# Performance work log

Measured on AMD Instinct MI355X. Metric: run time of the kernel, lower is better.

## Reference

```python
import jax, jax.numpy as jnp
import numpy as np

N_HEAD, D_MODEL, DQ, DK, DV = 16, 1024, 64, 64, 64
B, LQ, LK = 2, 2048, 2048
EPS = 1e-3


def setup_inputs() -> dict:
    key = jax.random.key(0)
    ks = jax.random.split(key, 8)
    v = jax.random.normal(ks[0], (B, LK, D_MODEL), jnp.float32)
    k = jax.random.normal(ks[1], (B, LK, D_MODEL), jnp.float32)
    q = jax.random.normal(ks[2], (B, LQ, D_MODEL), jnp.float32)
    mask = jax.random.randint(ks[3], (B, LQ, LK), 0, 2).astype(bool)
    # xavier_normal for [n_head, d_model, d*]: fan_in=d_model, fan_out=d* (per torch, last two dims)
    def xav(kk, shape):
        std = np.sqrt(2.0 / (shape[-2] + shape[-1]))
        return jax.random.normal(kk, shape, jnp.float32) * std
    w_q = xav(ks[4], (N_HEAD, D_MODEL, DQ))
    w_k = xav(ks[5], (N_HEAD, D_MODEL, DK))
    w_v = xav(ks[6], (N_HEAD, D_MODEL, DV))
    # output linear: torch default init; use uniform(-1/sqrt(fan_in), ..)
    fan_in = N_HEAD * DV
    bound = 1.0 / np.sqrt(fan_in)
    kw, kb = jax.random.split(ks[7])
    w_o = jax.random.uniform(kw, (fan_in, D_MODEL), jnp.float32, -bound, bound)
    b_o = jax.random.uniform(kb, (D_MODEL,), jnp.float32, -bound, bound)
    gamma = jnp.ones((D_MODEL,), jnp.float32)
    beta = jnp.zeros((D_MODEL,), jnp.float32)
    return {"v": v, "k": k, "q": q, "mask": mask, "w_q": w_q, "w_k": w_k,
            "w_v": w_v, "w_o": w_o, "b_o": b_o, "gamma": gamma, "beta": beta}


def _layer_norm(x, gamma, beta):
    mean = jnp.mean(x, axis=-1, keepdims=True)
    # torch.std default is unbiased (ddof=1); eps added to std (not var)
    std = jnp.std(x, axis=-1, keepdims=True, ddof=1)
    return (x - mean) / (std + EPS) * gamma + beta


def reference(v, k, q, mask, w_q, w_k, w_v, w_o, b_o, gamma, beta):
    residual = k  # source uses k as residual
    # per-head projections: [h, b, l, d*]
    qh = jnp.einsum('bld,hde->hble', q, w_q)
    kh = jnp.einsum('bld,hde->hble', k, w_k)
    vh = jnp.einsum('bld,hde->hble', v, w_v)
    scale = 1.0 / np.sqrt(DK)
    scores = jnp.einsum('hbqe,hbke->hbqk', qh, kh) * scale  # [h,b,Lq,Lk]
    scores = jnp.where(mask[None], -jnp.inf, scores)
    attn = jax.nn.softmax(scores, axis=-1)
    out = jnp.einsum('hbqk,hbke->hbqe', attn, vh)  # [h,b,Lq,dv]
    # cat(split(out, batch, dim=0), dim=-1): heads concatenated on last dim
    out = out.transpose(1, 2, 0, 3).reshape(out.shape[1], out.shape[2], -1)
    out = out @ w_o + b_o
    x = out + residual  # dropout is identity in eval
    return _layer_norm(x, gamma, beta)
```

## Files before the change

### kernel.cpp

```cpp
#include <hip/hip_runtime.h>
#include <math.h>

typedef __bf16 bf16_t;
typedef bf16_t bf16x8 __attribute__((ext_vector_type(8)));
typedef float  f32x4  __attribute__((ext_vector_type(4)));
typedef unsigned short u16;
typedef u16 ushortx4 __attribute__((ext_vector_type(4)));
typedef unsigned long long u64;

#define MFMA16(a, b, c) __builtin_amdgcn_mfma_f32_16x16x32_bf16((a), (b), (c), 0, 0, 0)

__device__ __forceinline__ u16 f2bf(float f) {
    unsigned int u = __float_as_uint(f);
    u = (u + 0x7fffu + ((u >> 16) & 1u)) >> 16;
    return (u16)u;
}

__device__ __forceinline__ float bf2f(unsigned int u) {
    return __uint_as_float(u << 16);
}

__device__ __forceinline__ void gld16(const u16* g, u16* l) {
    __builtin_amdgcn_global_load_lds(
        (const __attribute__((address_space(1))) void*)g,
        (__attribute__((address_space(3))) void*)l, 16, 0, 0);
}


__global__ __launch_bounds__(256) void k_cvt3(const float* __restrict__ q,
                                              const float* __restrict__ k,
                                              const float* __restrict__ v,
                                              u16* __restrict__ qb,
                                              u16* __restrict__ kb,
                                              u16* __restrict__ vb) {
    int i = blockIdx.x * 256 + threadIdx.x;
    int sel = blockIdx.y;
    const float* src = sel == 0 ? q : (sel == 1 ? k : v);
    u16* dst = sel == 0 ? qb : (sel == 1 ? kb : vb);
    float4 val = ((const float4*)src)[i];
    ushortx4 r;
    r[0] = f2bf(val.x); r[1] = f2bf(val.y); r[2] = f2bf(val.z); r[3] = f2bf(val.w);
    ((ushortx4*)dst)[i] = r;
}

__global__ __launch_bounds__(256) void k_tcvt3(const float* __restrict__ w_q,
                                               const float* __restrict__ w_k,
                                               const float* __restrict__ w_v,
                                               u16* __restrict__ wqt,
                                               u16* __restrict__ wkt,
                                               u16* __restrict__ wvt) {
    __shared__ float tile[32][33];
    int z = blockIdx.z, h = z & 15, sel = z >> 4;
    const float* src = (sel == 0 ? w_q : (sel == 1 ? w_k : w_v));
    u16* dst = (sel == 0 ? wqt : (sel == 1 ? wkt : wvt));
    int r0 = blockIdx.x * 32, c0 = blockIdx.y * 32;
    int tx = threadIdx.x & 31, ty = threadIdx.x >> 5;
    const float* s = src + ((size_t)h * 1024 + r0) * 64 + c0;
#pragma unroll
    for (int i = 0; i < 4; ++i) tile[ty + i * 8][tx] = s[(ty + i * 8) * 64 + tx];
    __syncthreads();
    u16* d = dst + ((size_t)h * 64 + c0) * 1024 + r0;
#pragma unroll
    for (int i = 0; i < 4; ++i) d[(ty + i * 8) * 1024 + tx] = f2bf(tile[tx][ty + i * 8]);
}

__global__ __launch_bounds__(256) void k_tcvt(const float* __restrict__ src,
                                              u16* __restrict__ dst, int R, int C) {
    __shared__ float tile[32][33];
    int r0 = blockIdx.x * 32, c0 = blockIdx.y * 32;
    int tx = threadIdx.x & 31, ty = threadIdx.x >> 5;
    const float* s = src + (size_t)r0 * C + c0;
#pragma unroll
    for (int i = 0; i < 4; ++i) tile[ty + i * 8][tx] = s[(ty + i * 8) * (size_t)C + tx];
    __syncthreads();
    u16* d = dst + (size_t)c0 * R + r0;
#pragma unroll
    for (int i = 0; i < 4; ++i) d[(ty + i * 8) * (size_t)R + tx] = f2bf(tile[tx][ty + i * 8]);
}

__global__ __launch_bounds__(256) void k_packmask(const int* __restrict__ mask,
                                                  u64* __restrict__ mask64) {
    int bid = blockIdx.x;
    int ktg = bid & 7, q4 = (bid >> 3) & 511, b = bid >> 12;
    int wave = threadIdx.x >> 6, lane = threadIdx.x & 63;
    int q = q4 * 4 + wave;
    const int* mp = mask + ((size_t)(b * 2048 + q)) * 2048 + ktg * 256 + lane;
#pragma unroll
    for (int i = 0; i < 4; ++i) {
        int m = mp[i * 64];
        u64 bal = __ballot(m != 0);
        if (lane == 0) mask64[((size_t)(b * 32 + ktg * 4 + i)) * 2048 + q] = bal;
    }
}

#define GEMM_CORE(Ablk, Bblk, ACC)                                                    \
    int c0 = wave * 2;                                                                \
    const u16* Ag0 = Ablk + (size_t)(c0 * 16 + l15) * 1024 + quad * 8;                \
    const u16* Ag1 = Ablk + (size_t)((c0 + 1) * 16 + l15) * 1024 + quad * 8;          \
    const u16* Bg0 = Bblk + (size_t)(c0 * 16 + l15) * 1024 + quad * 8;                \
    const u16* Bg1 = Bblk + (size_t)((c0 + 1) * 16 + l15) * 1024 + quad * 8;          \
    gld16(Ag0, As + c0 * 512); gld16(Ag1, As + (c0 + 1) * 512);                       \
    gld16(Bg0, Bs + c0 * 512); gld16(Bg1, Bs + (c0 + 1) * 512);                       \
    __syncthreads();                                                                  \
    int buf = 0;                                                                      \
    for (int ks = 0; ks < 32; ++ks) {                                                 \
        if (ks < 31) {                                                                \
            int k0 = (ks + 1) * 32;                                                   \
            gld16(Ag0 + k0, As + (buf ^ 1) * 4096 + c0 * 512);                        \
            gld16(Ag1 + k0, As + (buf ^ 1) * 4096 + (c0 + 1) * 512);                  \
            gld16(Bg0 + k0, Bs + (buf ^ 1) * 4096 + c0 * 512);                        \
            gld16(Bg1 + k0, Bs + (buf ^ 1) * 4096 + (c0 + 1) * 512);                  \
        }                                                                             \
        bf16x8 af[4], bfr[4];                                                         \
        _Pragma("unroll")                                                             \
        for (int i = 0; i < 4; ++i)                                                   \
            af[i] = *(const bf16x8*)(As + buf * 4096 + (wy * 4 + i) * 512 + lane * 8);\
        _Pragma("unroll")                                                             \
        for (int j = 0; j < 4; ++j)                                                   \
            bfr[j] = *(const bf16x8*)(Bs + buf * 4096 + (wx * 4 + j) * 512 + lane * 8);\
        _Pragma("unroll")                                                             \
        for (int i = 0; i < 4; ++i)                                                   \
            _Pragma("unroll")                                                         \
            for (int j = 0; j < 4; ++j) ACC[i][j] = MFMA16(af[i], bfr[j], ACC[i][j]); \
        __syncthreads();                                                              \
        buf ^= 1;                                                                     \
    }

__global__ __launch_bounds__(256) void k_proj(
    const u16* __restrict__ qb, const u16* __restrict__ kb, const u16* __restrict__ vb,
    const u16* __restrict__ wqt, const u16* __restrict__ wkt, const u16* __restrict__ wvt,
    u16* __restrict__ oq, u16* __restrict__ okh, u16* __restrict__ ovt) {
    __shared__ __align__(16) u16 smem[18432];
    u16* As = smem;
    u16* Bs = smem + 8192;
    int z = blockIdx.y, gx = blockIdx.x;
    int bm, bn;
    const u16 *A, *B;
    if (z == 0)      { bm = gx >> 3; bn = gx & 7; A = qb; B = wqt; }
    else if (z == 1) { bm = gx >> 3; bn = gx & 7; A = kb; B = wkt; }
    else             { bm = gx & 7; bn = gx >> 3; A = wvt; B = vb; }
    A += (size_t)bm * 128 * 1024;
    B += (size_t)bn * 128 * 1024;
    int tid = threadIdx.x, wave = tid >> 6, lane = tid & 63;
    int wy = wave >> 1, wx = wave & 1, l15 = lane & 15, quad = lane >> 4;
    f32x4 acc[4][4] = {};
    GEMM_CORE(A, B, acc)
    u16* ep = smem + wave * 4608;
    float mulf = (z == 0) ? 0.18033688011112042f : 1.0f;
#pragma unroll
    for (int i = 0; i < 4; ++i)
#pragma unroll
        for (int j = 0; j < 4; ++j)
#pragma unroll
            for (int r = 0; r < 4; ++r)
                ep[(i * 16 + quad * 4 + r) * 72 + j * 16 + l15] = f2bf(acc[i][j][r] * mulf);
    int rl = lane >> 3, cg = lane & 7;
    if (z < 2) {
        int hh = bn * 2 + wx;
        int m0 = bm * 128 + wy * 64;
        int bb = m0 >> 11, l0 = m0 & 2047;
        u16* O = (z ? okh : oq) + ((size_t)((hh * 2 + bb) * 2048 + l0)) * 64;
#pragma unroll
        for (int s = 0; s < 8; ++s) {
            int row = s * 8 + rl;
            uint4 v = *(const uint4*)(ep + row * 72 + cg * 8);
            *(uint4*)(O + (size_t)row * 64 + cg * 8) = v;
        }
    } else {
        int m0 = bm * 128 + wy * 64;
        int hh = m0 >> 6;
        int n0 = bn * 128 + wx * 64;
        int bb = n0 >> 11, l0 = n0 & 2047;
        u16* O = ovt + (size_t)(hh * 2 + bb) * 131072 + (size_t)(m0 & 63) * 2048 + l0;
#pragma unroll
        for (int s = 0; s < 8; ++s) {
            int row = s * 8 + rl;
            uint4 v = *(const uint4*)(ep + row * 72 + cg * 8);
            *(uint4*)(O + (size_t)row * 2048 + cg * 8) = v;
        }
    }
}

__global__ __launch_bounds__(512) void k_out(
    const u16* __restrict__ ao, const u16* __restrict__ wot,
    const float* __restrict__ bo, const float* __restrict__ resid,
    float* __restrict__ xb) {
    __shared__ __align__(16) u16 smem[18432];
    u16* As = smem;
    u16* Bs = smem + 8192;
    int gx = blockIdx.x, bm = gx >> 3, bn = gx & 7;
    const u16* A = ao + (size_t)bm * 128 * 1024;
    const u16* B = wot + (size_t)bn * 128 * 1024;
    int tid = threadIdx.x, wave = tid >> 6, lane = tid & 63;
    int wy = wave >> 2, wx = wave & 3, l15 = lane & 15, quad = lane >> 4;
    const u16* Ag = A + (size_t)(wave * 16 + l15) * 1024 + quad * 8;
    const u16* Bg = B + (size_t)(wave * 16 + l15) * 1024 + quad * 8;
    f32x4 acc[4][2] = {};
    gld16(Ag, As + wave * 512);
    gld16(Bg, Bs + wave * 512);
    __syncthreads();
    int buf = 0;
    for (int ks = 0; ks < 32; ++ks) {
        if (ks < 31) {
            int k0 = (ks + 1) * 32;
            gld16(Ag + k0, As + (buf ^ 1) * 4096 + wave * 512);
            gld16(Bg + k0, Bs + (buf ^ 1) * 4096 + wave * 512);
        }
        bf16x8 af[4], bfr[2];
#pragma unroll
        for (int i = 0; i < 4; ++i)
            af[i] = *(const bf16x8*)(As + buf * 4096 + (wy * 4 + i) * 512 + lane * 8);
#pragma unroll
        for (int j = 0; j < 2; ++j)
            bfr[j] = *(const bf16x8*)(Bs + buf * 4096 + (wx * 2 + j) * 512 + lane * 8);
#pragma unroll
        for (int i = 0; i < 4; ++i)
#pragma unroll
            for (int j = 0; j < 2; ++j) acc[i][j] = MFMA16(af[i], bfr[j], acc[i][j]);
        __syncthreads();
        buf ^= 1;
    }
    float* epf = (float*)smem + wave * 1152;
    int rl = lane >> 3, cg = lane & 7;
    int mbase = bm * 128 + wy * 64, nbase = bn * 128 + wx * 32;
#pragma unroll
    for (int cc = 0; cc < 2; ++cc) {
#pragma unroll
        for (int i2 = 0; i2 < 2; ++i2)
#pragma unroll
            for (int j = 0; j < 2; ++j)
#pragma unroll
                for (int r = 0; r < 4; ++r)
                    epf[(i2 * 16 + quad * 4 + r) * 36 + j * 16 + l15] =
                        acc[cc * 2 + i2][j][r];
#pragma unroll
        for (int s = 0; s < 4; ++s) {
            int row = s * 8 + rl;
            f32x4 v = *(const f32x4*)(epf + row * 36 + cg * 4);
            int m = mbase + cc * 32 + row, n = nbase + cg * 4;
            float4 rsd = *(const float4*)(resid + (size_t)m * 1024 + n);
            float4 bo4 = *(const float4*)(bo + n);
            float4 o;
            o.x = v[0] + bo4.x + rsd.x;
            o.y = v[1] + bo4.y + rsd.y;
            o.z = v[2] + bo4.z + rsd.z;
            o.w = v[3] + bo4.w + rsd.w;
            *(float4*)(xb + (size_t)m * 1024 + n) = o;
        }
    }
}

__global__ __launch_bounds__(512) void k_attn(
    const u16* __restrict__ qh, const u16* __restrict__ kh,
    const u16* __restrict__ vt, const u64* __restrict__ mask64,
    u16* __restrict__ po, float* __restrict__ pl) {
    int qt = blockIdx.x, hb = blockIdx.y, ksp = blockIdx.z;
    int b = hb & 1;
    int tid = threadIdx.x, wave = tid >> 6, lane = tid & 63;
    int l15 = lane & 15, quad = lane >> 4;

    __shared__ __align__(16) u16 Ks[2][4096], Vs[2][4096];
    __shared__ __align__(16) u16 Pb[8][16][72];

    int qrow0 = qt * 256 + wave * 32;
    const u16* Qp = qh + ((size_t)(hb * 2048) + qrow0 + l15) * 64 + quad * 8;
    bf16x8 qf[2][2];
    qf[0][0] = *(const bf16x8*)Qp;
    qf[0][1] = *(const bf16x8*)(Qp + 32);
    qf[1][0] = *(const bf16x8*)(Qp + 1024);
    qf[1][1] = *(const bf16x8*)(Qp + 1024 + 32);

    int rC = (wave >> 1) * 16 + l15, dC = (wave & 1) * 32 + quad * 8;
    const u16* Kg = kh + (size_t)hb * 131072 + (size_t)ksp * 65536 + (size_t)rC * 64 + dC;
    const u16* Vg = vt + (size_t)hb * 131072 + (size_t)rC * 2048 + ksp * 1024 + dC;
    const u64* Mp = mask64 + (size_t)b * 65536 + (size_t)ksp * 32768 + qrow0 + l15;

    float l_lane[2] = {0.f, 0.f};
    f32x4 o[2][4] = {};

    gld16(Kg, &Ks[0][wave * 512]);
    gld16(Vg, &Vs[0][wave * 512]);
    u64 mw0 = Mp[0], mw1 = Mp[16];
    __syncthreads();
    int buf = 0;
    for (int kt = 0; kt < 16; ++kt) {
        u64 mwn0 = 0, mwn1 = 0;
        if (kt < 15) {
            gld16(Kg + (size_t)(kt + 1) * 4096, &Ks[buf ^ 1][wave * 512]);
            gld16(Vg + (size_t)(kt + 1) * 64, &Vs[buf ^ 1][wave * 512]);
            mwn0 = Mp[(size_t)(kt + 1) * 2048];
            mwn1 = Mp[(size_t)(kt + 1) * 2048 + 16];
        }
        bf16x8 kf[8], vf[8];
#pragma unroll
        for (int c = 0; c < 8; ++c) kf[c] = *(const bf16x8*)&Ks[buf][c * 512 + lane * 8];
#pragma unroll
        for (int c = 0; c < 8; ++c) vf[c] = *(const bf16x8*)&Vs[buf][c * 512 + lane * 8];
#pragma unroll
        for (int hf = 0; hf < 2; ++hf) {
            u64 mw = hf ? mw1 : mw0;
            f32x4 st[4] = {};
#pragma unroll
            for (int t = 0; t < 4; ++t) {
                st[t] = MFMA16(kf[t * 2], qf[hf][0], st[t]);
                st[t] = MFMA16(kf[t * 2 + 1], qf[hf][1], st[t]);
            }
            unsigned int w0 = (unsigned int)(mw >> (quad * 4));
            unsigned int w1 = (unsigned int)(mw >> (32 + quad * 4));
#pragma unroll
            for (int r = 0; r < 4; ++r) {
                st[0][r] = ((w0 >> r) & 1u) ? -3e30f : st[0][r];
                st[1][r] = ((w0 >> (16 + r)) & 1u) ? -3e30f : st[1][r];
                st[2][r] = ((w1 >> r) & 1u) ? -3e30f : st[2][r];
                st[3][r] = ((w1 >> (16 + r)) & 1u) ? -3e30f : st[3][r];
            }
            float ll = 0.f;
#pragma unroll
            for (int t = 0; t < 4; ++t) {
                float p0 = __builtin_amdgcn_exp2f(st[t][0]);
                float p1 = __builtin_amdgcn_exp2f(st[t][1]);
                float p2 = __builtin_amdgcn_exp2f(st[t][2]);
                float p3 = __builtin_amdgcn_exp2f(st[t][3]);
                ll += (p0 + p1) + (p2 + p3);
                uint2 pk;
                pk.x = (__float_as_uint(p1) & 0xffff0000u) | (__float_as_uint(p0) >> 16);
                pk.y = (__float_as_uint(p3) & 0xffff0000u) | (__float_as_uint(p2) >> 16);
                *(uint2*)&Pb[wave][l15][t * 16 + quad * 4] = pk;
            }
            l_lane[hf] += ll;
#pragma unroll
            for (int kc = 0; kc < 2; ++kc) {
                bf16x8 pf = *(const bf16x8*)&Pb[wave][l15][kc * 32 + quad * 8];
#pragma unroll
                for (int t = 0; t < 4; ++t)
                    o[hf][t] = MFMA16(pf, vf[t * 2 + kc], o[hf][t]);
            }
        }
        mw0 = mwn0; mw1 = mwn1;
        __syncthreads();
        buf ^= 1;
    }
    size_t rowbase = ((size_t)ksp * 32 + hb) * 2048 + qrow0;
    int rl = lane >> 3, cg = lane & 7;
#pragma unroll
    for (int hf = 0; hf < 2; ++hf) {
        float ls = l_lane[hf];
        ls += __shfl_xor(ls, 16, 64);
        ls += __shfl_xor(ls, 32, 64);
        if (quad == 0) pl[rowbase + hf * 16 + l15] = ls;
#pragma unroll
        for (int t = 0; t < 4; ++t)
#pragma unroll
            for (int r = 0; r < 4; ++r)
                Pb[wave][quad * 4 + r][t * 16 + l15] = f2bf(o[hf][t][r]);
#pragma unroll
        for (int s = 0; s < 2; ++s) {
            int row = s * 8 + rl;
            uint4 v = *(const uint4*)&Pb[wave][row][cg * 8];
            *(uint4*)(po + (rowbase + hf * 16 + row) * 64 + cg * 8) = v;
        }
    }
}

__global__ __launch_bounds__(256) void k_amerge(const u16* __restrict__ po,
                                                const float* __restrict__ pl,
                                                u16* __restrict__ ao) {
    int bid = blockIdx.x;
    int hb = bid >> 6, rc = bid & 63;
    int h = hb >> 1, b = hb & 1;
    int tid = threadIdx.x;
    int r = tid >> 3, c = tid & 7;
    int row = rc * 32 + r;
    size_t i0 = ((size_t)hb * 2048 + row) * 64 + c * 8;
    uint4 a0 = *(const uint4*)(po + i0);
    uint4 a1 = *(const uint4*)(po + i0 + 4194304);
    float l0 = pl[(size_t)hb * 2048 + row];
    float l1 = pl[65536 + (size_t)hb * 2048 + row];
    float inv = 1.0f / (l0 + l1);
    unsigned int* pa0 = (unsigned int*)&a0;
    unsigned int* pa1 = (unsigned int*)&a1;
    uint4 out;
    unsigned int* po_ = (unsigned int*)&out;
#pragma unroll
    for (int i = 0; i < 4; ++i) {
        float lo = (bf2f(pa0[i] & 0xffffu) + bf2f(pa1[i] & 0xffffu)) * inv;
        float hi = (bf2f(pa0[i] >> 16) + bf2f(pa1[i] >> 16)) * inv;
        po_[i] = (unsigned int)f2bf(lo) | ((unsigned int)f2bf(hi) << 16);
    }
    *(uint4*)(ao + ((size_t)(b * 2048 + row)) * 1024 + h * 64 + c * 8) = out;
}

__global__ __launch_bounds__(256) void k_ln(const float* __restrict__ x,
                                            const float* __restrict__ gamma,
                                            const float* __restrict__ beta,
                                            float* __restrict__ out) {
    int row = blockIdx.x;
    const float* xr = x + (size_t)row * 1024;
    float4 v = ((const float4*)xr)[threadIdx.x];
    float s = v.x + v.y + v.z + v.w;
    float ss = v.x * v.x + v.y * v.y + v.z * v.z + v.w * v.w;
#pragma unroll
    for (int off = 32; off; off >>= 1) {
        s += __shfl_down(s, off, 64);
        ss += __shfl_down(ss, off, 64);
    }
    __shared__ float sb[8];
    int wave = threadIdx.x >> 6, lane = threadIdx.x & 63;
    if (lane == 0) { sb[wave] = s; sb[4 + wave] = ss; }
    __syncthreads();
    s = sb[0] + sb[1] + sb[2] + sb[3];
    ss = sb[4] + sb[5] + sb[6] + sb[7];
    float mean = s * (1.0f / 1024.0f);
    float var = fmaxf((ss - 1024.0f * mean * mean) * (1.0f / 1023.0f), 0.f);
    float inv = 1.0f / (sqrtf(var) + 1e-3f);
    float4 g = ((const float4*)gamma)[threadIdx.x];
    float4 bt = ((const float4*)beta)[threadIdx.x];
    float4 o;
    o.x = (v.x - mean) * inv * g.x + bt.x;
    o.y = (v.y - mean) * inv * g.y + bt.y;
    o.z = (v.z - mean) * inv * g.z + bt.z;
    o.w = (v.w - mean) * inv * g.w + bt.w;
    ((float4*)(out + (size_t)row * 1024))[threadIdx.x] = o;
}

extern "C" void kernel_launch(void* const* d_in, const int* in_sizes, int n_in,
                              void* d_out, int out_size, void* d_ws, size_t ws_size,
                              hipStream_t stream) {
    const float* v_in  = (const float*)d_in[0];
    const float* k_in  = (const float*)d_in[1];
    const float* q_in  = (const float*)d_in[2];
    const int*   mask  = (const int*)d_in[3];
    const float* w_q   = (const float*)d_in[4];
    const float* w_k   = (const float*)d_in[5];
    const float* w_v   = (const float*)d_in[6];
    const float* w_o   = (const float*)d_in[7];
    const float* b_o   = (const float*)d_in[8];
    const float* gamma = (const float*)d_in[9];
    const float* beta  = (const float*)d_in[10];
    float* out = (float*)d_out;

    char* ws = (char*)d_ws;
    const size_t MB = 1ull << 20;
    u16* qb  = (u16*)(ws + 0 * MB);
    u16* kb  = (u16*)(ws + 8 * MB);
    u16* vb  = (u16*)(ws + 16 * MB);
    u16* wqt = (u16*)(ws + 24 * MB);
    u16* wkt = (u16*)(ws + 26 * MB);
    u16* wvt = (u16*)(ws + 28 * MB);
    u16* wot = (u16*)(ws + 30 * MB);
    u16* qh  = (u16*)(ws + 32 * MB);
    u16* kh  = (u16*)(ws + 40 * MB);
    u16* vt  = (u16*)(ws + 48 * MB);
    u16* ao  = (u16*)(ws + 56 * MB);
    u64* mask64 = (u64*)(ws + 64 * MB);
    float* xb = (float*)(ws + 64 * MB);
    u16*   po = (u16*)(ws + 0 * MB);
    float* pl = (float*)(ws + 16 * MB);

    k_cvt3<<<dim3(4096, 3), dim3(256), 0, stream>>>(q_in, k_in, v_in, qb, kb, vb);
    k_tcvt3<<<dim3(32, 2, 48), dim3(256), 0, stream>>>(w_q, w_k, w_v, wqt, wkt, wvt);
    k_tcvt<<<dim3(32, 32), dim3(256), 0, stream>>>(w_o, wot, 1024, 1024);
    k_packmask<<<dim3(8192), dim3(256), 0, stream>>>(mask, mask64);
    k_proj<<<dim3(256, 3), dim3(256), 0, stream>>>(qb, kb, vb, wqt, wkt, wvt, qh, kh, vt);
    k_attn<<<dim3(8, 32, 2), dim3(512), 0, stream>>>(qh, kh, vt, mask64, po, pl);
    k_amerge<<<dim3(2048), dim3(256), 0, stream>>>(po, pl, ao);
    k_out<<<dim3(256), dim3(512), 0, stream>>>(ao, wot, b_o, k_in, xb);
    k_ln<<<dim3(4096), dim3(256), 0, stream>>>(xb, gamma, beta, out);
}
```

Measured before the change: 311.4 us.

## Merge prep kernels, shrink attention blocks with swizzled P, split-K output GEMM

Folds the four preprocessing launches (activation cast, mask packing, weight transposes) into two combined kernels to cut launch overhead. Attention blocks go from 512 to 256 threads covering 128 query rows, so the grid doubles, and the P/O staging buffer in shared memory gets an XOR swizzle to avoid bank conflicts. The output projection is split over K into two partial buffers, doubling its grid, and bias plus residual are added in the layernorm kernel. The cost is extra global traffic for the two fp32 partials and more blocks re-loading K/V tiles.

```diff
diff --git a/kernel.cpp b/kernel.cpp
--- a/kernel.cpp
+++ b/kernel.cpp
@@ -27,70 +27,71 @@
 }
 
 
-__global__ __launch_bounds__(256) void k_cvt3(const float* __restrict__ q,
+__global__ __launch_bounds__(256) void k_prep(const float* __restrict__ q,
                                               const float* __restrict__ k,
                                               const float* __restrict__ v,
+                                              const int* __restrict__ mask,
                                               u16* __restrict__ qb,
                                               u16* __restrict__ kb,
-                                              u16* __restrict__ vb) {
-    int i = blockIdx.x * 256 + threadIdx.x;
-    int sel = blockIdx.y;
-    const float* src = sel == 0 ? q : (sel == 1 ? k : v);
-    u16* dst = sel == 0 ? qb : (sel == 1 ? kb : vb);
-    float4 val = ((const float4*)src)[i];
-    ushortx4 r;
-    r[0] = f2bf(val.x); r[1] = f2bf(val.y); r[2] = f2bf(val.z); r[3] = f2bf(val.w);
-    ((ushortx4*)dst)[i] = r;
-}
-
-__global__ __launch_bounds__(256) void k_tcvt3(const float* __restrict__ w_q,
+                                              u16* __restrict__ vb,
+                                              u64* __restrict__ mask64) {
+    int bid = blockIdx.x;
+    if (bid < 12288) {
+        int sel = bid >> 12;
+        int i = (bid & 4095) * 256 + threadIdx.x;
+        const float* src = sel == 0 ? q : (sel == 1 ? k : v);
+        u16* dst = sel == 0 ? qb : (sel == 1 ? kb : vb);
+        float4 val = ((const float4*)src)[i];
+        ushortx4 r;
+        r[0] = f2bf(val.x); r[1] = f2bf(val.y); r[2] = f2bf(val.z); r[3] = f2bf(val.w);
+        ((ushortx4*)dst)[i] = r;
+    } else {
+        int b2 = bid - 12288;
+        int ktg = b2 & 7, q4 = (b2 >> 3) & 511, b = b2 >> 12;
+        int wave = threadIdx.x >> 6, lane = threadIdx.x & 63;
+        int qq = q4 * 4 + wave;
+        const int* mp = mask + ((size_t)(b * 2048 + qq)) * 2048 + ktg * 256 + lane;
+#pragma unroll
+        for (int i = 0; i < 4; ++i) {
+            int m = mp[i * 64];
+            u64 bal = __ballot(m != 0);
+            if (lane == 0) mask64[((size_t)(b * 32 + ktg * 4 + i)) * 2048 + qq] = bal;
+        }
+    }
+}
+
+__global__ __launch_bounds__(256) void k_prepw(const float* __restrict__ w_q,
                                                const float* __restrict__ w_k,
                                                const float* __restrict__ w_v,
+                                               const float* __restrict__ w_o,
                                                u16* __restrict__ wqt,
                                                u16* __restrict__ wkt,
-                                               u16* __restrict__ wvt) {
+                                               u16* __restrict__ wvt,
+                                               u16* __restrict__ wot) {
     __shared__ float tile[32][33];
-    int z = blockIdx.z, h = z & 15, sel = z >> 4;
-    const float* src = (sel == 0 ? w_q : (sel == 1 ? w_k : w_v));
-    u16* dst = (sel == 0 ? wqt : (sel == 1 ? wkt : wvt));
-    int r0 = blockIdx.x * 32, c0 = blockIdx.y * 32;
+    int bid = blockIdx.x;
+    const float* src;
+    u16* dst;
+    int r0, c0, R, C;
+    if (bid < 3072) {
+        int x = bid & 31, y = (bid >> 5) & 1, z = bid >> 6;
+        int h = z & 15, sel = z >> 4;
+        src = (sel == 0 ? w_q : (sel == 1 ? w_k : w_v)) + (size_t)h * 65536;
+        dst = (sel == 0 ? wqt : (sel == 1 ? wkt : wvt)) + (size_t)h * 65536;
+        r0 = x * 32; c0 = y * 32; R = 1024; C = 64;
+    } else {
+        int t = bid - 3072;
+        r0 = (t & 31) * 32; c0 = (t >> 5) * 32; R = 1024; C = 1024;
+        src = w_o; dst = wot;
+    }
     int tx = threadIdx.x & 31, ty = threadIdx.x >> 5;
-    const float* s = src + ((size_t)h * 1024 + r0) * 64 + c0;
-#pragma unroll
-    for (int i = 0; i < 4; ++i) tile[ty + i * 8][tx] = s[(ty + i * 8) * 64 + tx];
-    __syncthreads();
-    u16* d = dst + ((size_t)h * 64 + c0) * 1024 + r0;
-#pragma unroll
-    for (int i = 0; i < 4; ++i) d[(ty + i * 8) * 1024 + tx] = f2bf(tile[tx][ty + i * 8]);
-}
-
-__global__ __launch_bounds__(256) void k_tcvt(const float* __restrict__ src,
-                                              u16* __restrict__ dst, int R, int C) {
-    __shared__ float tile[32][33];
-    int r0 = blockIdx.x * 32, c0 = blockIdx.y * 32;
-    int tx = threadIdx.x & 31, ty = threadIdx.x >> 5;
-    const float* s = src + (size_t)r0 * C + c0;
+    const float* s = src + ((size_t)r0) * C + c0;
 #pragma unroll
     for (int i = 0; i < 4; ++i) tile[ty + i * 8][tx] = s[(ty + i * 8) * (size_t)C + tx];
     __syncthreads();
-    u16* d = dst + (size_t)c0 * R + r0;
+    u16* d = dst + ((size_t)c0) * R + r0;
 #pragma unroll
     for (int i = 0; i < 4; ++i) d[(ty + i * 8) * (size_t)R + tx] = f2bf(tile[tx][ty + i * 8]);
-}
-
-__global__ __launch_bounds__(256) void k_packmask(const int* __restrict__ mask,
-                                                  u64* __restrict__ mask64) {
-    int bid = blockIdx.x;
-    int ktg = bid & 7, q4 = (bid >> 3) & 511, b = bid >> 12;
-    int wave = threadIdx.x >> 6, lane = threadIdx.x & 63;
-    int q = q4 * 4 + wave;
-    const int* mp = mask + ((size_t)(b * 2048 + q)) * 2048 + ktg * 256 + lane;
-#pragma unroll
-    for (int i = 0; i < 4; ++i) {
-        int m = mp[i * 64];
-        u64 bal = __ballot(m != 0);
-        if (lane == 0) mask64[((size_t)(b * 32 + ktg * 4 + i)) * 2048 + q] = bal;
-    }
 }
 
 #define GEMM_CORE(Ablk, Bblk, ACC)                                                    \
@@ -181,76 +182,7 @@
     }
 }
 
-__global__ __launch_bounds__(512) void k_out(
-    const u16* __restrict__ ao, const u16* __restrict__ wot,
-    const float* __restrict__ bo, const float* __restrict__ resid,
-    float* __restrict__ xb) {
-    __shared__ __align__(16) u16 smem[18432];
-    u16* As = smem;
-    u16* Bs = smem + 8192;
-    int gx = blockIdx.x, bm = gx >> 3, bn = gx & 7;
-    const u16* A = ao + (size_t)bm * 128 * 1024;
-    const u16* B = wot + (size_t)bn * 128 * 1024;
-    int tid = threadIdx.x, wave = tid >> 6, lane = tid & 63;
-    int wy = wave >> 2, wx = wave & 3, l15 = lane & 15, quad = lane >> 4;
-    const u16* Ag = A + (size_t)(wave * 16 + l15) * 1024 + quad * 8;
-    const u16* Bg = B + (size_t)(wave * 16 + l15) * 1024 + quad * 8;
-    f32x4 acc[4][2] = {};
-    gld16(Ag, As + wave * 512);
-    gld16(Bg, Bs + wave * 512);
-    __syncthreads();
-    int buf = 0;
-    for (int ks = 0; ks < 32; ++ks) {
-        if (ks < 31) {
-            int k0 = (ks + 1) * 32;
-            gld16(Ag + k0, As + (buf ^ 1) * 4096 + wave * 512);
-            gld16(Bg + k0, Bs + (buf ^ 1) * 4096 + wave * 512);
-        }
-        bf16x8 af[4], bfr[2];
-#pragma unroll
-        for (int i = 0; i < 4; ++i)
-            af[i] = *(const bf16x8*)(As + buf * 4096 + (wy * 4 + i) * 512 + lane * 8);
-#pragma unroll
-        for (int j = 0; j < 2; ++j)
-            bfr[j] = *(const bf16x8*)(Bs + buf * 4096 + (wx * 2 + j) * 512 + lane * 8);
-#pragma unroll
-        for (int i = 0; i < 4; ++i)
-#pragma unroll
-            for (int j = 0; j < 2; ++j) acc[i][j] = MFMA16(af[i], bfr[j], acc[i][j]);
-        __syncthreads();
-        buf ^= 1;
-    }
-    float* epf = (float*)smem + wave * 1152;
-    int rl = lane >> 3, cg = lane & 7;
-    int mbase = bm * 128 + wy * 64, nbase = bn * 128 + wx * 32;
-#pragma unroll
-    for (int cc = 0; cc < 2; ++cc) {
-#pragma unroll
-        for (int i2 = 0; i2 < 2; ++i2)
-#pragma unroll
-            for (int j = 0; j < 2; ++j)
-#pragma unroll
-                for (int r = 0; r < 4; ++r)
-                    epf[(i2 * 16 + quad * 4 + r) * 36 + j * 16 + l15] =
-                        acc[cc * 2 + i2][j][r];
-#pragma unroll
-        for (int s = 0; s < 4; ++s) {
-            int row = s * 8 + rl;
-            f32x4 v = *(const f32x4*)(epf + row * 36 + cg * 4);
-            int m = mbase + cc * 32 + row, n = nbase + cg * 4;
-            float4 rsd = *(const float4*)(resid + (size_t)m * 1024 + n);
-            float4 bo4 = *(const float4*)(bo + n);
-            float4 o;
-            o.x = v[0] + bo4.x + rsd.x;
-            o.y = v[1] + bo4.y + rsd.y;
-            o.z = v[2] + bo4.z + rsd.z;
-            o.w = v[3] + bo4.w + rsd.w;
-            *(float4*)(xb + (size_t)m * 1024 + n) = o;
-        }
-    }
-}
-
-__global__ __launch_bounds__(512) void k_attn(
+__global__ __launch_bounds__(256) void k_attn(
     const u16* __restrict__ qh, const u16* __restrict__ kh,
     const u16* __restrict__ vt, const u64* __restrict__ mask64,
     u16* __restrict__ po, float* __restrict__ pl) {
@@ -260,9 +192,9 @@
     int l15 = lane & 15, quad = lane >> 4;
 
     __shared__ __align__(16) u16 Ks[2][4096], Vs[2][4096];
-    __shared__ __align__(16) u16 Pb[8][16][72];
-
-    int qrow0 = qt * 256 + wave * 32;
+    __shared__ __align__(16) u16 Pb[4][1024];
+
+    int qrow0 = qt * 128 + wave * 32;
     const u16* Qp = qh + ((size_t)(hb * 2048) + qrow0 + l15) * 64 + quad * 8;
     bf16x8 qf[2][2];
     qf[0][0] = *(const bf16x8*)Qp;
@@ -270,24 +202,33 @@
     qf[1][0] = *(const bf16x8*)(Qp + 1024);
     qf[1][1] = *(const bf16x8*)(Qp + 1024 + 32);
 
-    int rC = (wave >> 1) * 16 + l15, dC = (wave & 1) * 32 + quad * 8;
-    const u16* Kg = kh + (size_t)hb * 131072 + (size_t)ksp * 65536 + (size_t)rC * 64 + dC;
-    const u16* Vg = vt + (size_t)hb * 131072 + (size_t)rC * 2048 + ksp * 1024 + dC;
+    int c0 = wave * 2;
+    const u16* Kg0 = kh + (size_t)hb * 131072 + (size_t)ksp * 65536 +
+                     (size_t)(wave * 16 + l15) * 64 + quad * 8;
+    const u16* Kg1 = Kg0 + 32;
+    const u16* Vg0 = vt + (size_t)hb * 131072 + (size_t)(wave * 16 + l15) * 2048 +
+                     ksp * 1024 + quad * 8;
+    const u16* Vg1 = Vg0 + 32;
     const u64* Mp = mask64 + (size_t)b * 65536 + (size_t)ksp * 32768 + qrow0 + l15;
 
     float l_lane[2] = {0.f, 0.f};
     f32x4 o[2][4] = {};
 
-    gld16(Kg, &Ks[0][wave * 512]);
-    gld16(Vg, &Vs[0][wave * 512]);
+    gld16(Kg0, &Ks[0][c0 * 512]);
+    gld16(Kg1, &Ks[0][(c0 + 1) * 512]);
+    gld16(Vg0, &Vs[0][c0 * 512]);
+    gld16(Vg1, &Vs[0][(c0 + 1) * 512]);
     u64 mw0 = Mp[0], mw1 = Mp[16];
     __syncthreads();
     int buf = 0;
+    int swz = (l15 & 7) << 3;
     for (int kt = 0; kt < 16; ++kt) {
         u64 mwn0 = 0, mwn1 = 0;
         if (kt < 15) {
-            gld16(Kg + (size_t)(kt + 1) * 4096, &Ks[buf ^ 1][wave * 512]);
-            gld16(Vg + (size_t)(kt + 1) * 64, &Vs[buf ^ 1][wave * 512]);
+            gld16(Kg0 + (size_t)(kt + 1) * 4096, &Ks[buf ^ 1][c0 * 512]);
+            gld16(Kg1 + (size_t)(kt + 1) * 4096, &Ks[buf ^ 1][(c0 + 1) * 512]);
+            gld16(Vg0 + (size_t)(kt + 1) * 64, &Vs[buf ^ 1][c0 * 512]);
+            gld16(Vg1 + (size_t)(kt + 1) * 64, &Vs[buf ^ 1][(c0 + 1) * 512]);
             mwn0 = Mp[(size_t)(kt + 1) * 2048];
             mwn1 = Mp[(size_t)(kt + 1) * 2048 + 16];
         }
@@ -325,12 +266,15 @@
                 uint2 pk;
                 pk.x = (__float_as_uint(p1) & 0xffff0000u) | (__float_as_uint(p0) >> 16);
                 pk.y = (__float_as_uint(p3) & 0xffff0000u) | (__float_as_uint(p2) >> 16);
-                *(uint2*)&Pb[wave][l15][t * 16 + quad * 4] = pk;
+                int g = t * 2 + (quad >> 1);
+                int phys = l15 * 64 + (((g << 3) ^ swz)) + (quad & 1) * 4;
+                *(uint2*)&Pb[wave][phys] = pk;
             }
             l_lane[hf] += ll;
 #pragma unroll
             for (int kc = 0; kc < 2; ++kc) {
-                bf16x8 pf = *(const bf16x8*)&Pb[wave][l15][kc * 32 + quad * 8];
+                int g = kc * 4 + quad;
+                bf16x8 pf = *(const bf16x8*)&Pb[wave][l15 * 64 + (((g << 3) ^ swz))];
 #pragma unroll
                 for (int t = 0; t < 4; ++t)
                     o[hf][t] = MFMA16(pf, vf[t * 2 + kc], o[hf][t]);
@@ -351,12 +295,16 @@
 #pragma unroll
         for (int t = 0; t < 4; ++t)
 #pragma unroll
-            for (int r = 0; r < 4; ++r)
-                Pb[wave][quad * 4 + r][t * 16 + l15] = f2bf(o[hf][t][r]);
+            for (int r = 0; r < 4; ++r) {
+                int row = quad * 4 + r, col = t * 16 + l15;
+                int g = col >> 3;
+                Pb[wave][row * 64 + (((g ^ (row & 7)) << 3)) + (col & 7)] =
+                    f2bf(o[hf][t][r]);
+            }
 #pragma unroll
         for (int s = 0; s < 2; ++s) {
             int row = s * 8 + rl;
-            uint4 v = *(const uint4*)&Pb[wave][row][cg * 8];
+            uint4 v = *(const uint4*)&Pb[wave][row * 64 + ((cg ^ (row & 7)) << 3)];
             *(uint4*)(po + (rowbase + hf * 16 + row) * 64 + cg * 8) = v;
         }
     }
@@ -390,13 +338,87 @@
     *(uint4*)(ao + ((size_t)(b * 2048 + row)) * 1024 + h * 64 + c * 8) = out;
 }
 
-__global__ __launch_bounds__(256) void k_ln(const float* __restrict__ x,
+__global__ __launch_bounds__(512) void k_out(
+    const u16* __restrict__ ao, const u16* __restrict__ wot,
+    float* __restrict__ xp0, float* __restrict__ xp1) {
+    __shared__ __align__(16) u16 smem[18432];
+    u16* As = smem;
+    u16* Bs = smem + 8192;
+    int gx = blockIdx.x, bm = gx >> 3, bn = gx & 7;
+    int ksp = blockIdx.y;
+    const u16* A = ao + (size_t)bm * 128 * 1024 + ksp * 512;
+    const u16* B = wot + (size_t)bn * 128 * 1024 + ksp * 512;
+    float* xp = ksp ? xp1 : xp0;
+    int tid = threadIdx.x, wave = tid >> 6, lane = tid & 63;
+    int wy = wave >> 2, wx = wave & 3, l15 = lane & 15, quad = lane >> 4;
+    const u16* Ag = A + (size_t)(wave * 16 + l15) * 1024 + quad * 8;
+    const u16* Bg = B + (size_t)(wave * 16 + l15) * 1024 + quad * 8;
+    f32x4 acc[4][2] = {};
+    gld16(Ag, As + wave * 512);
+    gld16(Bg, Bs + wave * 512);
+    __syncthreads();
+    int buf = 0;
+    for (int ks = 0; ks < 16; ++ks) {
+        if (ks < 15) {
+            int k0 = (ks + 1) * 32;
+            gld16(Ag + k0, As + (buf ^ 1) * 4096 + wave * 512);
+            gld16(Bg + k0, Bs + (buf ^ 1) * 4096 + wave * 512);
+        }
+        bf16x8 af[4], bfr[2];
+#pragma unroll
+        for (int i = 0; i < 4; ++i)
+            af[i] = *(const bf16x8*)(As + buf * 4096 + (wy * 4 + i) * 512 + lane * 8);
+#pragma unroll
+        for (int j = 0; j < 2; ++j)
+            bfr[j] = *(const bf16x8*)(Bs + buf * 4096 + (wx * 2 + j) * 512 + lane * 8);
+#pragma unroll
+        for (int i = 0; i < 4; ++i)
+#pragma unroll
+            for (int j = 0; j < 2; ++j) acc[i][j] = MFMA16(af[i], bfr[j], acc[i][j]);
+        __syncthreads();
+        buf ^= 1;
+    }
+    float* epf = (float*)smem + wave * 1152;
+    int rl = lane >> 3, cg = lane & 7;
+    int mbase = bm * 128 + wy * 64, nbase = bn * 128 + wx * 32;
+#pragma unroll
+    for (int cc = 0; cc < 2; ++cc) {
+#pragma unroll
+        for (int i2 = 0; i2 < 2; ++i2)
+#pragma unroll
+            for (int j = 0; j < 2; ++j)
+#pragma unroll
+                for (int r = 0; r < 4; ++r)
+                    epf[(i2 * 16 + quad * 4 + r) * 36 + j * 16 + l15] =
+                        acc[cc * 2 + i2][j][r];
+#pragma unroll
+        for (int s = 0; s < 4; ++s) {
+            int row = s * 8 + rl;
+            f32x4 v = *(const f32x4*)(epf + row * 36 + cg * 4);
+            int m = mbase + cc * 32 + row, n = nbase + cg * 4;
+            *(f32x4*)(xp + (size_t)m * 1024 + n) = v;
+        }
+    }
+}
+
+__global__ __launch_bounds__(256) void k_ln(const float* __restrict__ xp0,
+                                            const float* __restrict__ xp1,
+                                            const float* __restrict__ resid,
+                                            const float* __restrict__ bo,
                                             const float* __restrict__ gamma,
                                             const float* __restrict__ beta,
                                             float* __restrict__ out) {
     int row = blockIdx.x;
-    const float* xr = x + (size_t)row * 1024;
-    float4 v = ((const float4*)xr)[threadIdx.x];
+    size_t base = (size_t)row * 256;
+    float4 a0 = ((const float4*)xp0)[base + threadIdx.x];
+    float4 a1 = ((const float4*)xp1)[base + threadIdx.x];
+    float4 rs = ((const float4*)resid)[base + threadIdx.x];
+    float4 b4 = ((const float4*)bo)[threadIdx.x];
+    float4 v;
+    v.x = a0.x + a1.x + rs.x + b4.x;
+    v.y = a0.y + a1.y + rs.y + b4.y;
+    v.z = a0.z + a1.z + rs.z + b4.z;
+    v.w = a0.w + a1.w + rs.w + b4.w;
     float s = v.x + v.y + v.z + v.w;
     float ss = v.x * v.x + v.y * v.y + v.z * v.z + v.w * v.w;
 #pragma unroll
@@ -420,7 +442,7 @@
     o.y = (v.y - mean) * inv * g.y + bt.y;
     o.z = (v.z - mean) * inv * g.z + bt.z;
     o.w = (v.w - mean) * inv * g.w + bt.w;
-    ((float4*)(out + (size_t)row * 1024))[threadIdx.x] = o;
+    ((float4*)(out))[base + threadIdx.x] = o;
 }
 
 extern "C" void kernel_launch(void* const* d_in, const int* in_sizes, int n_in,
@@ -453,17 +475,18 @@
     u16* vt  = (u16*)(ws + 48 * MB);
     u16* ao  = (u16*)(ws + 56 * MB);
     u64* mask64 = (u64*)(ws + 64 * MB);
-    float* xb = (float*)(ws + 64 * MB);
     u16*   po = (u16*)(ws + 0 * MB);
     float* pl = (float*)(ws + 16 * MB);
-
-    k_cvt3<<<dim3(4096, 3), dim3(256), 0, stream>>>(q_in, k_in, v_in, qb, kb, vb);
-    k_tcvt3<<<dim3(32, 2, 48), dim3(256), 0, stream>>>(w_q, w_k, w_v, wqt, wkt, wvt);
-    k_tcvt<<<dim3(32, 32), dim3(256), 0, stream>>>(w_o, wot, 1024, 1024);
-    k_packmask<<<dim3(8192), dim3(256), 0, stream>>>(mask, mask64);
+    float* xp0 = (float*)(ws + 32 * MB);
+    float* xp1 = (float*)(ws + 64 * MB);
+
+    k_prep<<<dim3(20480), dim3(256), 0, stream>>>(q_in, k_in, v_in, mask,
+                                                  qb, kb, vb, mask64);
+    k_prepw<<<dim3(4096), dim3(256), 0, stream>>>(w_q, w_k, w_v, w_o,
+                                                  wqt, wkt, wvt, wot);
     k_proj<<<dim3(256, 3), dim3(256), 0, stream>>>(qb, kb, vb, wqt, wkt, wvt, qh, kh, vt);
-    k_attn<<<dim3(8, 32, 2), dim3(512), 0, stream>>>(qh, kh, vt, mask64, po, pl);
+    k_attn<<<dim3(16, 32, 2), dim3(256), 0, stream>>>(qh, kh, vt, mask64, po, pl);
     k_amerge<<<dim3(2048), dim3(256), 0, stream>>>(po, pl, ao);
-    k_out<<<dim3(256), dim3(512), 0, stream>>>(ao, wot, b_o, k_in, xb);
-    k_ln<<<dim3(4096), dim3(256), 0, stream>>>(xb, gamma, beta, out);
-}
+    k_out<<<dim3(256, 2), dim3(512), 0, stream>>>(ao, wot, xp0, xp1);
+    k_ln<<<dim3(4096), dim3(256), 0, stream>>>(xp0, xp1, k_in, b_o, gamma, beta, out);
+}
```

Result: no change. 308.9 us (-0.8%).
